# Kernel optimization log

Hardware: AMD Instinct MI355X
Metric: run time of the kernel (lower is better)

Reference implementation:

```python
import jax, jax.numpy as jnp
import numpy as np

NU, NI, DIN, DOUT, NS, E = 100000, 100000, 128, 128, 5, 500000


def setup_inputs() -> dict:
    key = jax.random.key(0)
    ks = jax.random.split(key, 9)
    scale = 1.0 / np.sqrt(DIN)
    return {
        "user_inputs": jax.random.normal(ks[0], (NU, DIN), jnp.float32),
        "item_inputs": jax.random.normal(ks[1], (NI, DIN), jnp.float32),
        "weight": jax.random.normal(ks[2], (DIN, DOUT, NS), jnp.float32) * scale,
        "u_rows": jax.random.randint(ks[3], (NS, E), 0, NU),
        "u_cols": jax.random.randint(ks[4], (NS, E), 0, NI),
        "u_vals": jax.random.uniform(ks[5], (NS, E), jnp.float32),
        "i_rows": jax.random.randint(ks[6], (NS, E), 0, NI),
        "i_cols": jax.random.randint(ks[7], (NS, E), 0, NU),
        "i_vals": jax.random.uniform(ks[8], (NS, E), jnp.float32),
    }


def _spmm(rows, cols, vals, dense, n_rows):
    # COO sparse [n_rows, n_cols] @ dense [n_cols, d] -> [n_rows, d]
    msgs = vals[:, None] * dense[cols]  # [E, d]
    return jax.ops.segment_sum(msgs, rows, num_segments=n_rows)


def reference(user_inputs, item_inputs, weight, u_rows, u_cols, u_vals, i_rows, i_cols, i_vals):
    n_users = user_inputs.shape[0]
    n_items = item_inputs.shape[0]
    num_support = weight.shape[-1]
    w = jnp.zeros(weight.shape[:2], weight.dtype)
    user_hidden = jnp.zeros((n_users, weight.shape[1]), weight.dtype)
    item_hidden = jnp.zeros((n_items, weight.shape[1]), weight.dtype)
    for i in range(num_support):  # fixed small structural loop (5 rating levels)
        w = w + weight[..., i]            # cumulative weight sum, as in original
        tmp_u = user_inputs @ w           # [NU, DOUT]
        tmp_v = item_inputs @ w           # [NI, DOUT]
        user_hidden = user_hidden + _spmm(u_rows[i], u_cols[i], u_vals[i], tmp_v, n_users)
        item_hidden = item_hidden + _spmm(i_rows[i], i_cols[i], i_vals[i], tmp_u, n_items)
    return jax.nn.relu(user_hidden), jax.nn.relu(item_hidden)
```

## Files before the change

kernel.cpp:

```cpp
#include <hip/hip_runtime.h>

#define R_     100000
#define NSUP   5
#define EDGES  500000
#define D_     128
#define ND     (NSUP * D_)
#define BR     64
#define PPS2   ((R_ + BR - 1) / BR)
#define CAP2   512

#define EPB    4096
#define BPS    123
#define NB_C   196
#define CST    128
#define CROWS  (NB_C + 1)
#define ECAP   2944

#define PPB    12500
#define BTB    160

using short8 = __attribute__((ext_vector_type(8))) short;
using f32x4  = __attribute__((ext_vector_type(4))) float;

static __device__ __forceinline__ float bf2f_lo(unsigned p) { return __uint_as_float(p << 16); }
static __device__ __forceinline__ float bf2f_hi(unsigned p) { return __uint_as_float(p & 0xffff0000u); }
static __device__ __forceinline__ unsigned short f2bf(float x) {
    unsigned u = __float_as_uint(x);
    return (unsigned short)((u + 0x7fffu + ((u >> 16) & 1u)) >> 16);
}

__global__ __launch_bounds__(512) void pp_k(const float* __restrict__ user_in,
                                            const float* __restrict__ item_in,
                                            const float* __restrict__ w,
                                            const int* __restrict__ u_rows,
                                            const int* __restrict__ u_cols,
                                            const float* __restrict__ u_vals,
                                            const int* __restrict__ i_rows,
                                            const int* __restrict__ i_cols,
                                            const float* __restrict__ i_vals,
                                            unsigned short* __restrict__ srcb,
                                            unsigned short* __restrict__ bt,
                                            int* __restrict__ coff,
                                            uint2* __restrict__ cedge2) {
    __shared__ uint2 estage[EPB];
    __shared__ int   hist[NB_C];
    __shared__ int   wsum[8];

    int b = blockIdx.x, tid = threadIdx.x;
    if (b < PPB) {
        int side = b / 6250;
        int t = (b - side * 6250) * 512 + tid;
        const float* src = side ? user_in : item_in;
        float4 v = *(const float4*)(src + (size_t)t * 4);
        ushort4 o;
        o.x = f2bf(v.x); o.y = f2bf(v.y); o.z = f2bf(v.z); o.w = f2bf(v.w);
        *(ushort4*)(srcb + (size_t)side * (R_ * D_) + (size_t)t * 4) = o;
        return;
    }
    if (b < PPB + BTB) {
        int t = (b - PPB) * 512 + tid;
        int o = t / ND;
        int kk = t - o * ND;
        int i = kk >> 7, d = kk & 127;
        float s = 0.f;
        for (int j = 0; j <= i; j++) s += w[(d * D_ + o) * NSUP + j];
        bt[t] = f2bf(s);
        return;
    }
    int q = b - (PPB + BTB);
    int seg = q / BPS;
    int bb  = q - seg * BPS;
    int side = seg / NSUP;
    int sup  = seg - side * NSUP;
    const int*   rows = side ? i_rows : u_rows;
    const int*   cols = side ? i_cols : u_cols;
    const float* vals = side ? i_vals : u_vals;
    int e0 = bb * EPB;
    int ecnt = EDGES - e0; if (ecnt > EPB) ecnt = EPB;
    size_t gb = (size_t)sup * EDGES + e0;

    if (tid < NB_C) hist[tid] = 0;
    __syncthreads();
    for (int e = tid; e < ecnt; e += 512)
        atomicAdd(&hist[rows[gb + e] >> 9], 1);
    __syncthreads();
    int cnt = (tid < NB_C) ? hist[tid] : 0;
    int lane = tid & 63, wv = tid >> 6;
    int s = cnt;
#pragma unroll
    for (int off = 1; off < 64; off <<= 1) {
        int u = __shfl_up(s, off, 64);
        if (lane >= off) s += u;
    }
    if (lane == 63) wsum[wv] = s;
    __syncthreads();
    int woff = 0;
#pragma unroll
    for (int k = 0; k < 8; k++) woff += (k < wv) ? wsum[k] : 0;
    int ex = woff + s - cnt;
    if (tid < NB_C) {
        coff[(size_t)(seg * CROWS + tid) * CST + bb] = ex;
        hist[tid] = ex;
    }
    if (tid == 0) coff[(size_t)(seg * CROWS + NB_C) * CST + bb] = ecnt;
    __syncthreads();
    for (int e = tid; e < ecnt; e += 512) {
        int r = rows[gb + e];
        int pos = atomicAdd(&hist[r >> 9], 1);
        uint2 E;
        E.x = (unsigned)cols[gb + e] | ((unsigned)(r & 511) << 17);
        E.y = __float_as_uint(vals[gb + e]);
        estage[pos] = E;
    }
    __syncthreads();
    size_t cbase = (size_t)(seg * BPS + bb) * EPB;
    for (int e = tid; e < ecnt; e += 512) cedge2[cbase + e] = estage[e];
}

__global__ __launch_bounds__(512) void binsort_k(const int* __restrict__ coff,
                                                 const uint2* __restrict__ cedge2,
                                                 uint2* __restrict__ cedge3,
                                                 int* __restrict__ rtab) {
    __shared__ uint2 estage[ECAP];
    __shared__ unsigned short perm[ECAP];
    __shared__ int hs[512];
    __shared__ int cur[512];
    __shared__ int rstart[BPS + 1];
    __shared__ int ro0[BPS];
    __shared__ int wsum[8];

    int q = blockIdx.x;
    int seg = q / NB_C;
    int c   = q - seg * NB_C;
    int side = seg / NSUP;
    int sup  = seg - side * NSUP;
    int tid = threadIdx.x;
    int lane = tid & 63, wv = tid >> 6;

    cur[tid] = 0;
    if (wv == 0) {
        const int* crow = coff + (size_t)(seg * CROWS + c) * CST;
        int j0 = lane * 2, j1 = j0 + 1;
        int o0 = 0, o1 = 0, c0 = 0, c1 = 0;
        if (j0 < BPS) { o0 = crow[j0]; c0 = crow[j0 + CST] - o0; }
        if (j1 < BPS) { o1 = crow[j1]; c1 = crow[j1 + CST] - o1; }
        int sc = c0 + c1;
        int s = sc;
#pragma unroll
        for (int off = 1; off < 64; off <<= 1) {
            int u = __shfl_up(s, off, 64);
            if (lane >= off) s += u;
        }
        int ex = s - sc;
        if (j0 < BPS) { rstart[j0] = ex;      ro0[j0] = o0; }
        if (j1 < BPS) { rstart[j1] = ex + c0; ro0[j1] = o1; }
        if (lane == 63) rstart[BPS] = s;
    }
    __syncthreads();
    int n = rstart[BPS]; if (n > ECAP) n = ECAP;
    if (tid < 4 * BPS) {
        int rb = tid >> 2, j0 = tid & 3;
        int rs = rstart[rb];
        int cntr = rstart[rb + 1] - rs;
        const uint2* src = cedge2 + (size_t)(seg * BPS + rb) * EPB + ro0[rb];
        for (int j = j0; j < cntr; j += 4) {
            int pos = rs + j;
            if (pos < ECAP) estage[pos] = src[j];
        }
    }
    __syncthreads();
    for (int e = tid; e < n; e += 512)
        atomicAdd(&cur[(estage[e].x >> 17) & 511], 1);
    __syncthreads();
    int cnt = cur[tid];
    int s = cnt;
#pragma unroll
    for (int off = 1; off < 64; off <<= 1) {
        int u = __shfl_up(s, off, 64);
        if (lane >= off) s += u;
    }
    if (lane == 63) wsum[wv] = s;
    __syncthreads();
    int woff = 0;
#pragma unroll
    for (int k = 0; k < 8; k++) woff += (k < wv) ? wsum[k] : 0;
    int sinc = woff + s;
    hs[tid] = sinc;
    cur[tid] = sinc - cnt;
    __syncthreads();
    int b_ = tid >> 6;
    int gbin = c * 8 + b_;
    if (gbin < PPS2) {
        int binst = b_ ? hs[(b_ << 6) - 1] : 0;
        int srel = sinc - binst; if (srel > CAP2) srel = CAP2;
        rtab[((size_t)(side * PPS2 + gbin)) * (NSUP * BR) + sup * BR + (tid & 63)] = srel;
    }
    for (int e = tid; e < n; e += 512) {
        int pos = atomicAdd(&cur[(estage[e].x >> 17) & 511], 1);
        perm[pos] = (unsigned short)e;
    }
    __syncthreads();
    size_t segbase = (size_t)(side * NSUP + sup) * PPS2;
    for (int ep = tid; ep < n; ep += 512) {
        uint2 E = estage[perm[ep]];
        int rl = (E.x >> 17) & 511;
        int b2 = rl >> 6;
        int gb2 = c * 8 + b2;
        int binst = b2 ? hs[(b2 << 6) - 1] : 0;
        int wpos = ep - binst;
        if (wpos < CAP2 && gb2 < PPS2)
            cedge3[(segbase + gb2) * CAP2 + wpos] = E;
    }
}

__global__ __launch_bounds__(512, 8) void fused_k(const uint2* __restrict__ cedge3,
                                                  const int* __restrict__ rtab,
                                                  const unsigned short* __restrict__ srcb,
                                                  const unsigned short* __restrict__ BT,
                                                  float* __restrict__ out) {
    __shared__ unsigned short stile[BR * D_];
    __shared__ uint2 eds5[NSUP * CAP2];
    __shared__ int rsc_all[NSUP * BR];

    int side = blockIdx.x / PPS2;
    int bin  = blockIdx.x - side * PPS2;
    const unsigned short* srcbf = srcb + (size_t)side * (R_ * D_);
    float* outp = out + (size_t)side * R_ * D_;

    int tid = threadIdx.x;
    int wid = tid >> 6, lane = tid & 63;
    int g = lane >> 4, l16 = lane & 15;

    size_t rbase = ((size_t)(side * PPS2 + bin)) * (NSUP * BR);
    if (tid < NSUP * BR) rsc_all[tid] = rtab[rbase + tid];
#pragma unroll
    for (int i = 0; i < NSUP; i++) {
        int n = rtab[rbase + i * BR + 63]; if (n > CAP2) n = CAP2;
        const uint2* ebase = cedge3 + (size_t)((side * NSUP + i) * PPS2 + bin) * CAP2;
        for (int e = tid; e < n; e += 512) eds5[i * CAP2 + e] = ebase[e];
    }

    f32x4 acc[4];
#pragma unroll
    for (int rt = 0; rt < 4; rt++) acc[rt] = (f32x4){0.f, 0.f, 0.f, 0.f};

    __syncthreads();

    for (int i = 0; i < NSUP; i++) {
        const uint2* eds = eds5 + i * CAP2;
        for (int rq = wid; rq < 16; rq += 8) {
            int r = rq * 4 + g;
            int s0 = r ? rsc_all[i * BR + r - 1] : 0;
            int e2 = rsc_all[i * BR + r];
            float a0 = 0.f, a1 = 0.f, a2 = 0.f, a3 = 0.f;
            float a4 = 0.f, a5 = 0.f, a6 = 0.f, a7 = 0.f;
            int e = s0;
            for (; e + 3 < e2; e += 4) {
                uint2 E0 = eds[e], E1 = eds[e + 1], E2 = eds[e + 2], E3 = eds[e + 3];
                const uint4 p0 = *(const uint4*)(srcbf + (size_t)(E0.x & 0x1FFFFu) * D_ + l16 * 8);
                const uint4 p1 = *(const uint4*)(srcbf + (size_t)(E1.x & 0x1FFFFu) * D_ + l16 * 8);
                const uint4 p2 = *(const uint4*)(srcbf + (size_t)(E2.x & 0x1FFFFu) * D_ + l16 * 8);
                const uint4 p3 = *(const uint4*)(srcbf + (size_t)(E3.x & 0x1FFFFu) * D_ + l16 * 8);
                float v0 = __uint_as_float(E0.y), v1 = __uint_as_float(E1.y);
                float v2 = __uint_as_float(E2.y), v3 = __uint_as_float(E3.y);
                a0 += v0 * bf2f_lo(p0.x); a1 += v0 * bf2f_hi(p0.x);
                a2 += v0 * bf2f_lo(p0.y); a3 += v0 * bf2f_hi(p0.y);
                a4 += v0 * bf2f_lo(p0.z); a5 += v0 * bf2f_hi(p0.z);
                a6 += v0 * bf2f_lo(p0.w); a7 += v0 * bf2f_hi(p0.w);
                a0 += v1 * bf2f_lo(p1.x); a1 += v1 * bf2f_hi(p1.x);
                a2 += v1 * bf2f_lo(p1.y); a3 += v1 * bf2f_hi(p1.y);
                a4 += v1 * bf2f_lo(p1.z); a5 += v1 * bf2f_hi(p1.z);
                a6 += v1 * bf2f_lo(p1.w); a7 += v1 * bf2f_hi(p1.w);
                a0 += v2 * bf2f_lo(p2.x); a1 += v2 * bf2f_hi(p2.x);
                a2 += v2 * bf2f_lo(p2.y); a3 += v2 * bf2f_hi(p2.y);
                a4 += v2 * bf2f_lo(p2.z); a5 += v2 * bf2f_hi(p2.z);
                a6 += v2 * bf2f_lo(p2.w); a7 += v2 * bf2f_hi(p2.w);
                a0 += v3 * bf2f_lo(p3.x); a1 += v3 * bf2f_hi(p3.x);
                a2 += v3 * bf2f_lo(p3.y); a3 += v3 * bf2f_hi(p3.y);
                a4 += v3 * bf2f_lo(p3.z); a5 += v3 * bf2f_hi(p3.z);
                a6 += v3 * bf2f_lo(p3.w); a7 += v3 * bf2f_hi(p3.w);
            }
            for (; e < e2; e++) {
                uint2 E = eds[e];
                const uint4 pk = *(const uint4*)(srcbf + (size_t)(E.x & 0x1FFFFu) * D_ + l16 * 8);
                float vv = __uint_as_float(E.y);
                a0 += vv * bf2f_lo(pk.x); a1 += vv * bf2f_hi(pk.x);
                a2 += vv * bf2f_lo(pk.y); a3 += vv * bf2f_hi(pk.y);
                a4 += vv * bf2f_lo(pk.z); a5 += vv * bf2f_hi(pk.z);
                a6 += vv * bf2f_lo(pk.w); a7 += vv * bf2f_hi(pk.w);
            }
            uint4 P;
            P.x = ((unsigned)f2bf(a1) << 16) | f2bf(a0);
            P.y = ((unsigned)f2bf(a3) << 16) | f2bf(a2);
            P.z = ((unsigned)f2bf(a5) << 16) | f2bf(a4);
            P.w = ((unsigned)f2bf(a7) << 16) | f2bf(a6);
            int boff = r * 256 + ((l16 * 16) ^ ((r & 7) << 4));
            *(uint4*)((char*)stile + boff) = P;
        }
        __syncthreads();

        const unsigned short* btp = BT + (size_t)(wid * 16 + l16) * ND + i * D_;
#pragma unroll
        for (int cc = 0; cc < 4; cc++) {
            short8 bfr = *(const short8*)(btp + cc * 32 + g * 8);
#pragma unroll
            for (int rt = 0; rt < 4; rt++) {
                int row = rt * 16 + l16;
                int boff = row * 256 + ((cc * 64 + g * 16) ^ ((row & 7) << 4));
                short8 afr = *(const short8*)((const char*)stile + boff);
                acc[rt] = __builtin_amdgcn_mfma_f32_16x16x32_bf16(afr, bfr, acc[rt], 0, 0, 0);
            }
        }
        __syncthreads();
    }

    float* ltile = (float*)stile;
#pragma unroll
    for (int half = 0; half < 2; half++) {
#pragma unroll
        for (int rt2 = 0; rt2 < 2; rt2++) {
#pragma unroll
            for (int rr = 0; rr < 4; rr++) {
                int lrow = rt2 * 16 + g * 4 + rr;
                float v = acc[half * 2 + rt2][rr];
                v = v > 0.f ? v : 0.f;
                *(float*)((char*)ltile + lrow * 512 +
                          (((wid * 16 + l16) * 4) ^ ((lrow & 7) << 4))) = v;
            }
        }
        __syncthreads();
#pragma unroll
        for (int s = 0; s < 2; s++) {
            int idx = tid + s * 512;
            int lrow = idx >> 5, c4 = idx & 31;
            int grow = bin * BR + half * 32 + lrow;
            if (grow < R_) {
                float4 v = *(const float4*)((const char*)ltile + lrow * 512 +
                                            ((c4 * 16) ^ ((lrow & 7) << 4)));
                *(float4*)(outp + (size_t)grow * D_ + c4 * 4) = v;
            }
        }
        __syncthreads();
    }
}

extern "C" void kernel_launch(void* const* d_in, const int* in_sizes, int n_in,
                              void* d_out, int out_size, void* d_ws, size_t ws_size,
                              hipStream_t stream) {
    const float* user_in = (const float*)d_in[0];
    const float* item_in = (const float*)d_in[1];
    const float* weight  = (const float*)d_in[2];
    const int* u_rows = (const int*)d_in[3];
    const int* u_cols = (const int*)d_in[4];
    const float* u_vals = (const float*)d_in[5];
    const int* i_rows = (const int*)d_in[6];
    const int* i_cols = (const int*)d_in[7];
    const float* i_vals = (const float*)d_in[8];
    float* out = (float*)d_out;

    char* ws = (char*)d_ws;
    unsigned short* srcb = (unsigned short*)(ws);
    unsigned short* BT   = (unsigned short*)(ws + 51200000);
    uint2* cedge2        = (uint2*)         (ws + 51363840);
    int*   coff          = (int*)           (ws + 91668480);
    uint2* cedge3        = (uint2*)         (ws + 92677120);
    int*   rtab          = (int*)           (ws + 156697600);

    pp_k<<<PPB + BTB + 10 * BPS, 512, 0, stream>>>(user_in, item_in, weight,
                                                   u_rows, u_cols, u_vals,
                                                   i_rows, i_cols, i_vals,
                                                   srcb, BT, coff, cedge2);
    binsort_k<<<10 * NB_C, 512, 0, stream>>>(coff, cedge2, cedge3, rtab);
    fused_k<<<2 * PPS2, 512, 0, stream>>>(cedge3, rtab, srcb, BT, out);
}
```

Measured before the change: 494.9 us.

## Split fused gather-GEMM blocks into half-row-tile blocks of 256 threads

Each fused_k block now handles 32 of the 64 rows in a bin with 256 threads instead of all 64 rows with 512 threads, and the grid doubles to match. Each wave now computes a 32x32 output tile (2x2 MFMA tiles) instead of 64x16. Shared memory per block roughly halves (stile and edge staging), which should let more blocks fit per CU and reduce barrier stalls across the gather and MFMA phases. In exchange, each block still loads the full row-offset table, and B fragments are loaded twice across the two half-blocks.

```diff
diff --git a/kernel.cpp b/kernel.cpp
--- a/kernel.cpp
+++ b/kernel.cpp
@@ -8,6 +8,7 @@
 #define BR     64
 #define PPS2   ((R_ + BR - 1) / BR)
 #define CAP2   512
+#define HCAP   256
 
 #define EPB    4096
 #define BPS    123
@@ -213,17 +214,21 @@
     }
 }
 
-__global__ __launch_bounds__(512, 8) void fused_k(const uint2* __restrict__ cedge3,
+__global__ __launch_bounds__(256, 8) void fused_k(const uint2* __restrict__ cedge3,
                                                   const int* __restrict__ rtab,
                                                   const unsigned short* __restrict__ srcb,
                                                   const unsigned short* __restrict__ BT,
                                                   float* __restrict__ out) {
-    __shared__ unsigned short stile[BR * D_];
-    __shared__ uint2 eds5[NSUP * CAP2];
+    __shared__ unsigned short stile[32 * D_];
+    __shared__ uint2 eds5[NSUP * HCAP];
     __shared__ int rsc_all[NSUP * BR];
 
-    int side = blockIdx.x / PPS2;
-    int bin  = blockIdx.x - side * PPS2;
+    int bid = blockIdx.x;
+    int side = bid / (PPS2 * 2);
+    int rem  = bid - side * (PPS2 * 2);
+    int bin  = rem >> 1;
+    int half = rem & 1;
+    int hbase = half * 32;
     const unsigned short* srcbf = srcb + (size_t)side * (R_ * D_);
     float* outp = out + (size_t)side * R_ * D_;
 
@@ -232,26 +237,41 @@
     int g = lane >> 4, l16 = lane & 15;
 
     size_t rbase = ((size_t)(side * PPS2 + bin)) * (NSUP * BR);
-    if (tid < NSUP * BR) rsc_all[tid] = rtab[rbase + tid];
+    for (int j = tid; j < NSUP * BR; j += 256)
+        rsc_all[j] = rtab[rbase + j];
+    __syncthreads();
+
 #pragma unroll
     for (int i = 0; i < NSUP; i++) {
-        int n = rtab[rbase + i * BR + 63]; if (n > CAP2) n = CAP2;
-        const uint2* ebase = cedge3 + (size_t)((side * NSUP + i) * PPS2 + bin) * CAP2;
-        for (int e = tid; e < n; e += 512) eds5[i * CAP2 + e] = ebase[e];
-    }
-
-    f32x4 acc[4];
-#pragma unroll
-    for (int rt = 0; rt < 4; rt++) acc[rt] = (f32x4){0.f, 0.f, 0.f, 0.f};
+        int st0 = hbase ? rsc_all[i * BR + hbase - 1] : 0;
+        int end = rsc_all[i * BR + hbase + 31];
+        int cnt = end - st0;
+        if (cnt > HCAP) cnt = HCAP;
+        if (cnt < 0) cnt = 0;
+        const uint2* ebase = cedge3 + (size_t)((side * NSUP + i) * PPS2 + bin) * CAP2 + st0;
+        for (int e = tid; e < cnt; e += 256) eds5[i * HCAP + e] = ebase[e];
+    }
+
+    f32x4 acc[2][2];
+#pragma unroll
+    for (int rt = 0; rt < 2; rt++)
+#pragma unroll
+        for (int nt = 0; nt < 2; nt++)
+            acc[rt][nt] = (f32x4){0.f, 0.f, 0.f, 0.f};
 
     __syncthreads();
 
     for (int i = 0; i < NSUP; i++) {
-        const uint2* eds = eds5 + i * CAP2;
-        for (int rq = wid; rq < 16; rq += 8) {
+        const uint2* eds = eds5 + i * HCAP;
+        int st0 = hbase ? rsc_all[i * BR + hbase - 1] : 0;
+#pragma unroll
+        for (int rq = wid; rq < 8; rq += 4) {
             int r = rq * 4 + g;
-            int s0 = r ? rsc_all[i * BR + r - 1] : 0;
-            int e2 = rsc_all[i * BR + r];
+            int gr = hbase + r;
+            int s0 = (gr ? rsc_all[i * BR + gr - 1] : 0) - st0;
+            int e2 = rsc_all[i * BR + gr] - st0;
+            if (s0 < 0) s0 = 0;
+            if (e2 > HCAP) e2 = HCAP;
             float a0 = 0.f, a1 = 0.f, a2 = 0.f, a3 = 0.f;
             float a4 = 0.f, a5 = 0.f, a6 = 0.f, a7 = 0.f;
             int e = s0;
@@ -299,16 +319,20 @@
         }
         __syncthreads();
 
-        const unsigned short* btp = BT + (size_t)(wid * 16 + l16) * ND + i * D_;
+        const unsigned short* btp0 = BT + (size_t)(wid * 32 + l16) * ND + i * D_;
 #pragma unroll
         for (int cc = 0; cc < 4; cc++) {
-            short8 bfr = *(const short8*)(btp + cc * 32 + g * 8);
-#pragma unroll
-            for (int rt = 0; rt < 4; rt++) {
-                int row = rt * 16 + l16;
-                int boff = row * 256 + ((cc * 64 + g * 16) ^ ((row & 7) << 4));
-                short8 afr = *(const short8*)((const char*)stile + boff);
-                acc[rt] = __builtin_amdgcn_mfma_f32_16x16x32_bf16(afr, bfr, acc[rt], 0, 0, 0);
+#pragma unroll
+            for (int nt = 0; nt < 2; nt++) {
+                short8 bfr = *(const short8*)(btp0 + (size_t)(nt * 16) * ND + cc * 32 + g * 8);
+#pragma unroll
+                for (int rt = 0; rt < 2; rt++) {
+                    int row = rt * 16 + l16;
+                    int boff = row * 256 + ((cc * 64 + g * 16) ^ ((row & 7) << 4));
+                    short8 afr = *(const short8*)((const char*)stile + boff);
+                    acc[rt][nt] = __builtin_amdgcn_mfma_f32_16x16x32_bf16(afr, bfr,
+                                                                          acc[rt][nt], 0, 0, 0);
+                }
             }
         }
         __syncthreads();
@@ -316,27 +340,27 @@
 
     float* ltile = (float*)stile;
 #pragma unroll
-    for (int half = 0; half < 2; half++) {
-#pragma unroll
-        for (int rt2 = 0; rt2 < 2; rt2++) {
+    for (int p = 0; p < 2; p++) {
+#pragma unroll
+        for (int nt = 0; nt < 2; nt++) {
 #pragma unroll
             for (int rr = 0; rr < 4; rr++) {
-                int lrow = rt2 * 16 + g * 4 + rr;
-                float v = acc[half * 2 + rt2][rr];
+                int lr = g * 4 + rr;
+                float v = acc[p][nt][rr];
                 v = v > 0.f ? v : 0.f;
-                *(float*)((char*)ltile + lrow * 512 +
-                          (((wid * 16 + l16) * 4) ^ ((lrow & 7) << 4))) = v;
+                int col = wid * 32 + nt * 16 + l16;
+                *(float*)((char*)ltile + lr * 512 + ((col * 4) ^ ((lr & 7) << 4))) = v;
             }
         }
         __syncthreads();
 #pragma unroll
         for (int s = 0; s < 2; s++) {
-            int idx = tid + s * 512;
-            int lrow = idx >> 5, c4 = idx & 31;
-            int grow = bin * BR + half * 32 + lrow;
+            int idx = tid + s * 256;
+            int lr = idx >> 5, c4 = idx & 31;
+            int grow = bin * BR + hbase + p * 16 + lr;
             if (grow < R_) {
-                float4 v = *(const float4*)((const char*)ltile + lrow * 512 +
-                                            ((c4 * 16) ^ ((lrow & 7) << 4)));
+                float4 v = *(const float4*)((const char*)ltile + lr * 512 +
+                                            ((c4 * 16) ^ ((lr & 7) << 4)));
                 *(float4*)(outp + (size_t)grow * D_ + c4 * 4) = v;
             }
         }
@@ -371,5 +395,5 @@
                                                    i_rows, i_cols, i_vals,
                                                    srcb, BT, coff, cedge2);
     binsort_k<<<10 * NB_C, 512, 0, stream>>>(coff, cedge2, cedge3, rtab);
-    fused_k<<<2 * PPS2, 512, 0, stream>>>(cedge3, rtab, srcb, BT, out);
-}
+    fused_k<<<2 * PPS2 * 2, 256, 0, stream>>>(cedge3, rtab, srcb, BT, out);
+}
```

Result: slower. 510.5 us (+3.2%).
